# Kernel optimization log

Measured on AMD Instinct MI355X. Metric: run time of the kernel, lower is better.

The kernel has to match this reference:

```python
import jax, jax.numpy as jnp
import numpy as np

NEG_SLOPE = 0.01  # torch nn.LeakyReLU default
K_NN = 3          # PyG knn_interpolate default


def lrelu(v):
    return jax.nn.leaky_relu(v, NEG_SLOPE)


def mpl(x, ei, We, be, Wn, bn_):
    # MeshGraphNets-style message passing: edge MLP on [x_src||x_dst],
    # sum-aggregate at dst, node MLP on [x||agg].
    src, dst = ei[0], ei[1]
    m = lrelu(jnp.concatenate([x[src], x[dst]], axis=-1) @ We + be)   # [E, Co]
    agg = jax.ops.segment_sum(m, dst, num_segments=x.shape[0])        # [N, Co]
    return lrelu(jnp.concatenate([x, agg], axis=-1) @ Wn + bn_)


def knn_interpolate(x_c, pos_c, pos_f):
    # PyG knn_interpolate: inverse-squared-distance weighted k-NN average.
    d2 = jnp.sum((pos_f[:, None, :] - pos_c[None, :, :]) ** 2, axis=-1)  # [Nf, Nc]
    neg_d2, idx = jax.lax.top_k(-d2, K_NN)                               # [Nf, k]
    w = 1.0 / (-neg_d2 + 1e-16)
    xg = x_c[idx]                                                        # [Nf, k, C]
    return jnp.sum(w[..., None] * xg, axis=1) / jnp.sum(w, axis=1, keepdims=True)


def batch_norm(x, gamma, beta, eps=1e-5):
    # training-mode BatchNorm over the flattened node dim (PyG BatchNorm)
    mu = x.mean(axis=0)
    var = x.var(axis=0)
    return (x - mu) * jax.lax.rsqrt(var + eps) * gamma + beta


def setup_inputs() -> dict:
    key = jax.random.key(0)
    ks = jax.random.split(key, 20)
    B, Nc, Nf, D = 4, 2048, 8192, 3
    Cin, Cout = 128, 128
    Ch = Cout // 2
    Ec, Ef = 16384, 65536

    def w(k, shape):
        return jax.random.normal(k, shape, jnp.float32) / np.float32(np.sqrt(shape[0]))

    inp = {
        "x": jax.random.normal(ks[0], (B, Nc, Cin), jnp.float32),
        "weights": jax.random.uniform(ks[1], (B, Nc, 1), dtype=jnp.float32),
        "pos": jax.random.uniform(ks[2], (B, Nf, D), dtype=jnp.float32),
        # mpl1: Cin -> Cout//2 (coarse graph)
        "W1e": w(ks[3], (2 * Cin, Ch)), "b1e": jnp.zeros((Ch,), jnp.float32),
        "W1n": w(ks[4], (Cin + Ch, Ch)), "b1n": jnp.zeros((Ch,), jnp.float32),
        # mpl2: Cout//2 -> Cout (fine graph)
        "W2e": w(ks[5], (2 * Ch, Cout)), "b2e": jnp.zeros((Cout,), jnp.float32),
        "W2n": w(ks[6], (Ch + Cout, Cout)), "b2n": jnp.zeros((Cout,), jnp.float32),
        # mpl_skip: Cin -> Cout (fine graph)
        "Wse": w(ks[7], (2 * Cin, Cout)), "bse": jnp.zeros((Cout,), jnp.float32),
        "Wsn": w(ks[8], (Cin + Cout, Cout)), "bsn": jnp.zeros((Cout,), jnp.float32),
        "gamma": jnp.ones((Cout,), jnp.float32),
        "beta": jnp.zeros((Cout,), jnp.float32),
        # mask: indices of coarse nodes inside the fine node set (disjoint per graph)
        "mask": jnp.arange(B * Nc, dtype=jnp.int32).reshape(B, Nc),
        "e_coarse": jax.random.randint(ks[9], (B, 2, Ec), 0, Nc, jnp.int32),
        "e_fine": jax.random.randint(ks[10], (B, 2, Ef), 0, Nf, jnp.int32),
    }
    return inp


def reference(x, weights, pos, W1e, b1e, W1n, b1n, W2e, b2e, W2n, b2n,
              Wse, bse, Wsn, bsn, gamma, beta, mask, e_coarse, e_fine):
    B, Nf, _ = pos.shape

    def per_graph(xg, wg, posg, mg, ec, ef):
        pos_c = posg[mg]                                   # coarse positions
        # skip branch: up-pool then message passing on fine graph
        x_up = knn_interpolate(xg, pos_c, posg)            # [Nf, Cin]
        x_skip = mpl(x_up, ef, Wse, bse, Wsn, bsn)         # [Nf, Cout]
        # main branch: mpl on coarse graph, up-pool, mpl on fine graph
        x1 = mpl(xg, ec, W1e, b1e, W1n, b1n)               # [Nc, Cout//2]
        x1_up = knn_interpolate(x1, pos_c, posg)           # [Nf, Cout//2]
        x2 = mpl(x1_up, ef, W2e, b2e, W2n, b2n)            # [Nf, Cout]
        # Unpool node weights (scatter into zeros at mask rows)
        w_fine = jnp.zeros((Nf, wg.shape[-1]), wg.dtype).at[mg].set(wg)
        return x2 + x_skip, w_fine

    xs, w_fine = jax.vmap(per_graph)(x, weights, pos, mask, e_coarse, e_fine)
    C = xs.shape[-1]
    y = lrelu(batch_norm(xs.reshape(-1, C), gamma, beta)).reshape(xs.shape)
    return y, w_fine
```

## Files before the change

### kernel.cpp

```cpp
#include <hip/hip_runtime.h>
#include <hip/hip_bf16.h>
#include <cfloat>

#define B 4
#define NC 2048
#define NF 8192
#define CIN 128
#define CH 64
#define COUT 128
#define EC 16384
#define EF 65536
#define ZB 256

typedef __attribute__((ext_vector_type(8))) short short8v;
typedef __attribute__((ext_vector_type(4))) float f32x4;

__device__ __forceinline__ ushort f2b(float v) {
    __hip_bfloat16 h = __float2bfloat16(v);
    return *reinterpret_cast<ushort*>(&h);
}
__device__ __forceinline__ float b2f(ushort u) {
    __hip_bfloat16 h = *reinterpret_cast<__hip_bfloat16*>(&u);
    return __bfloat162float(h);
}

__global__ void count_all(const int* __restrict__ ec, const int* __restrict__ ef,
                          const int* __restrict__ mask, const float* __restrict__ pos,
                          int* __restrict__ cntC, int* __restrict__ cntF, int* __restrict__ cntZ,
                          int* __restrict__ inv,
                          const float* __restrict__ W2e, const float* __restrict__ W2n,
                          const float* __restrict__ Wse, const float* __restrict__ Wsn,
                          ushort* __restrict__ W2eT, ushort* __restrict__ W2nT,
                          ushort* __restrict__ WseT, ushort* __restrict__ WsnT) {
    const int b = blockIdx.y, z = blockIdx.z;
    const int i = blockIdx.x * 256 + threadIdx.x;
    if (z == 0) {
        if (i < EC) atomicAdd(&cntC[b * NC + ec[(size_t)b * 2 * EC + EC + i]], 1);
    } else if (z == 1) {
        if (i < EF) atomicAdd(&cntF[b * NF + ef[(size_t)b * 2 * EF + EF + i]], 1);
        if (i < NF) inv[(size_t)b * NF + i] = -1;
    } else if (z == 2) {
        if (i < NC) {
            int m = mask[b * NC + i];
            float pz = pos[((size_t)b * NF + m) * 3 + 2];
            int zb = min(max((int)(pz * (float)ZB), 0), ZB - 1);
            atomicAdd(&cntZ[b * ZB + zb], 1);
        }
    } else {
        const float* src; ushort* dst; int K2;
        switch (b) {
            case 0: src = W2e; dst = W2eT; K2 = 128; break;
            case 1: src = W2n; dst = W2nT; K2 = 192; break;
            case 2: src = Wse; dst = WseT; K2 = 256; break;
            default: src = Wsn; dst = WsnT; K2 = 256; break;
        }
        if (i < K2 * 128) {
            int n = i & 127, k = i >> 7;
            dst[(size_t)n * K2 + k] = f2b(src[i]);
        }
    }
}

template<int N, int OSTR, bool EXTRA>
__device__ __forceinline__ void scan_body(const int* __restrict__ cnt, int* __restrict__ offs,
                                          int* __restrict__ cur, int b, int* part) {
    const int tid = threadIdx.x;
    constexpr int PER = (N + 1023) / 1024;
    int local[PER];
    int s = 0;
    #pragma unroll
    for (int i = 0; i < PER; ++i) {
        int id = tid * PER + i;
        local[i] = s;
        if (id < N) s += cnt[b * N + id];
    }
    part[tid] = s;
    __syncthreads();
    for (int off = 1; off < 1024; off <<= 1) {
        int v = (tid >= off) ? part[tid - off] : 0;
        __syncthreads();
        part[tid] += v;
        __syncthreads();
    }
    int pre = tid ? part[tid - 1] : 0;
    #pragma unroll
    for (int i = 0; i < PER; ++i) {
        int id = tid * PER + i;
        if (id < N) {
            int o = pre + local[i];
            offs[b * OSTR + id] = o;
            cur[b * OSTR + id] = o;
        }
    }
    if (EXTRA && tid == 1023) offs[b * OSTR + N] = part[1023];
}

__global__ __launch_bounds__(1024) void scan_all(
    const int* __restrict__ cntC, int* __restrict__ offC, int* __restrict__ curC,
    const int* __restrict__ cntF, int* __restrict__ offF, int* __restrict__ curF,
    const int* __restrict__ cntZ, int* __restrict__ offZ, int* __restrict__ curZ) {
    __shared__ int part[1024];
    const int cfg = blockIdx.x >> 2;
    const int b = blockIdx.x & 3;
    if (cfg == 0)      scan_body<NC, NC, false>(cntC, offC, curC, b, part);
    else if (cfg == 1) scan_body<NF, NF, false>(cntF, offF, curF, b, part);
    else               scan_body<ZB, ZB + 1, true>(cntZ, offZ, curZ, b, part);
}

__global__ void fill_all(const int* __restrict__ ec, const int* __restrict__ ef,
                         const int* __restrict__ mask, const float* __restrict__ pos,
                         int* __restrict__ curC, int* __restrict__ curF, int* __restrict__ curZ,
                         int* __restrict__ csrC, int* __restrict__ csrF,
                         float4* __restrict__ sposg, int* __restrict__ inv) {
    const int b = blockIdx.y, z = blockIdx.z;
    const int i = blockIdx.x * 256 + threadIdx.x;
    if (z == 0) {
        if (i < EC) {
            const int* eb = ec + (size_t)b * 2 * EC;
            int src = eb[i], dst = eb[EC + i];
            int p = atomicAdd(&curC[b * NC + dst], 1);
            csrC[(size_t)b * EC + p] = src;
        }
    } else if (z == 1) {
        if (i < EF) {
            const int* eb = ef + (size_t)b * 2 * EF;
            int src = eb[i], dst = eb[EF + i];
            int p = atomicAdd(&curF[b * NF + dst], 1);
            csrF[(size_t)b * EF + p] = src;
        }
    } else {
        if (i < NC) {
            int m = mask[b * NC + i];
            const float* p = pos + ((size_t)b * NF + m) * 3;
            float px = p[0], py = p[1], pz = p[2];
            int zb = min(max((int)(pz * (float)ZB), 0), ZB - 1);
            int slot = atomicAdd(&curZ[b * (ZB + 1) + zb], 1);
            sposg[(size_t)b * NC + slot] = make_float4(px, py, pz, __int_as_float(i));
            inv[(size_t)b * NF + m] = b * NC + i;
        }
    }
}

__device__ __forceinline__ void ins3(float d, int c, float& d0, float& d1, float& d2,
                                     int& i0, int& i1, int& i2) {
    bool lt0 = d < d0, lt1 = d < d1, lt2 = d < d2;
    d2 = lt1 ? d1 : (lt2 ? d : d2);  i2 = lt1 ? i1 : (lt2 ? c : i2);
    d1 = lt0 ? d0 : (lt1 ? d : d1);  i1 = lt0 ? i0 : (lt1 ? c : i1);
    d0 = lt0 ? d  : d0;              i0 = lt0 ? c  : i0;
}
__device__ __forceinline__ void merge32(float& d0, float& d1, float& d2,
                                        int& i0, int& i1, int& i2) {
    #pragma unroll
    for (int off = 1; off <= 16; off <<= 1) {
        float od[3]; int oi[3];
        od[0] = __shfl_xor(d0, off); oi[0] = __shfl_xor(i0, off);
        od[1] = __shfl_xor(d1, off); oi[1] = __shfl_xor(i1, off);
        od[2] = __shfl_xor(d2, off); oi[2] = __shfl_xor(i2, off);
        #pragma unroll
        for (int j = 0; j < 3; ++j) ins3(od[j], oi[j], d0, d1, d2, i0, i1, i2);
    }
}

__global__ __launch_bounds__(256) void knn_interp(const float* __restrict__ pos,
                                                  const float4* __restrict__ sposg,
                                                  const int* __restrict__ offZ,
                                                  const float* __restrict__ xc,
                                                  int* __restrict__ idx,
                                                  float* __restrict__ wn,
                                                  ushort* __restrict__ xup) {
    const int b = blockIdx.y;
    const int tid = threadIdx.x;
    const int node = blockIdx.x * 8 + (tid >> 5);
    const int lane = tid & 31;
    const float* pf = pos + ((size_t)b * NF + node) * 3;
    const float px = pf[0], py = pf[1], pz = pf[2];
    const float4* sp = sposg + (size_t)b * NC;
    const int zb = min(max((int)(pz * (float)ZB), 0), ZB - 1);
    const int zlo = max(zb - 32, 0), zhi = min(zb + 32, ZB - 1);
    const int j0 = offZ[b * (ZB + 1) + zlo];
    const int j1 = offZ[b * (ZB + 1) + zhi + 1];
    float d0 = FLT_MAX, d1 = FLT_MAX, d2 = FLT_MAX;
    int i0 = 0, i1 = 0, i2 = 0;
    for (int j = j0 + lane; j < j1; j += 32) {
        float4 s = sp[j];
        float ddx = __fsub_rn(px, s.x);
        float ddy = __fsub_rn(py, s.y);
        float ddz = __fsub_rn(pz, s.z);
        float d = __fadd_rn(__fadd_rn(__fmul_rn(ddx, ddx), __fmul_rn(ddy, ddy)),
                            __fmul_rn(ddz, ddz));
        ins3(d, __float_as_int(s.w), d0, d1, d2, i0, i1, i2);
    }
    merge32(d0, d1, d2, i0, i1, i2);
    float bd = 1e30f;
    if (zlo > 0)      bd = fminf(bd, pz - (float)zlo * (1.0f / ZB));
    if (zhi < ZB - 1) bd = fminf(bd, (float)(zhi + 1) * (1.0f / ZB) - pz);
    bd *= 0.9999f;
    if (__any(d2 > bd * bd)) {
        d0 = d1 = d2 = FLT_MAX; i0 = i1 = i2 = 0;
        for (int j = lane; j < NC; j += 32) {
            float4 s = sp[j];
            float ddx = __fsub_rn(px, s.x);
            float ddy = __fsub_rn(py, s.y);
            float ddz = __fsub_rn(pz, s.z);
            float d = __fadd_rn(__fadd_rn(__fmul_rn(ddx, ddx), __fmul_rn(ddy, ddy)),
                                __fmul_rn(ddz, ddz));
            ins3(d, __float_as_int(s.w), d0, d1, d2, i0, i1, i2);
        }
        merge32(d0, d1, d2, i0, i1, i2);
    }
    float w0 = 1.0f / (d0 + 1e-16f);
    float w1 = 1.0f / (d1 + 1e-16f);
    float w2 = 1.0f / (d2 + 1e-16f);
    float inv = 1.0f / (w0 + w1 + w2);
    w0 *= inv; w1 *= inv; w2 *= inv;
    if (lane == 0) {
        size_t o = ((size_t)b * NF + node) * 3;
        idx[o] = i0; idx[o + 1] = i1; idx[o + 2] = i2;
        wn[o] = w0; wn[o + 1] = w1; wn[o + 2] = w2;
    }
    const float* xb = xc + (size_t)b * NC * CIN;
    float4 a = *(const float4*)&xb[(size_t)i0 * CIN + lane * 4];
    float4 bb = *(const float4*)&xb[(size_t)i1 * CIN + lane * 4];
    float4 cc = *(const float4*)&xb[(size_t)i2 * CIN + lane * 4];
    ushort4 u;
    u.x = f2b(w0 * a.x + w1 * bb.x + w2 * cc.x);
    u.y = f2b(w0 * a.y + w1 * bb.y + w2 * cc.y);
    u.z = f2b(w0 * a.z + w1 * bb.z + w2 * cc.z);
    u.w = f2b(w0 * a.w + w1 * bb.w + w2 * cc.w);
    *(ushort4*)&xup[((size_t)b * NF + node) * CIN + lane * 4] = u;
}

template<int S>
__global__ __launch_bounds__(256) void interp_b16(const float* __restrict__ xc,
                                                  const int* __restrict__ idx,
                                                  const float* __restrict__ wn,
                                                  ushort* __restrict__ out) {
    constexpr int C = 4 << S;
    const int b = blockIdx.y;
    const int node = blockIdx.x * (256 >> S) + (threadIdx.x >> S);
    const int lane = threadIdx.x & ((1 << S) - 1);
    size_t o = ((size_t)b * NF + node) * 3;
    int i0 = idx[o], i1 = idx[o + 1], i2 = idx[o + 2];
    float w0 = wn[o], w1 = wn[o + 1], w2 = wn[o + 2];
    const float* xb = xc + (size_t)b * NC * C;
    float4 a = *(const float4*)&xb[(size_t)i0 * C + lane * 4];
    float4 bb = *(const float4*)&xb[(size_t)i1 * C + lane * 4];
    float4 cc = *(const float4*)&xb[(size_t)i2 * C + lane * 4];
    ushort4 u;
    u.x = f2b(w0 * a.x + w1 * bb.x + w2 * cc.x);
    u.y = f2b(w0 * a.y + w1 * bb.y + w2 * cc.y);
    u.z = f2b(w0 * a.z + w1 * bb.z + w2 * cc.z);
    u.w = f2b(w0 * a.w + w1 * bb.w + w2 * cc.w);
    *(ushort4*)&out[((size_t)b * NF + node) * C + lane * 4] = u;
}

__global__ __launch_bounds__(256) void gemm_kernel(
    const float* __restrict__ A1, int K1, const float* __restrict__ A2, int K2,
    const float* __restrict__ W, const float* __restrict__ bias,
    float* __restrict__ Cmat, int M, int N, int flags,
    long sA1, long sA2, long sC) {
    __shared__ float As[16][64];
    __shared__ float Wsh[16][64];
    const int b = blockIdx.z;
    const int m0 = blockIdx.y * 64, n0 = blockIdx.x * 64;
    const int t = threadIdx.x;
    const int tx = t & 15, ty = t >> 4;
    float acc[4][4] = {};
    int kOff = 0;
    for (int s = 0; s < 2; ++s) {
        const float* A = (s == 0) ? A1 : A2;
        const int K = (s == 0) ? K1 : K2;
        const long sA = (s == 0) ? sA1 : sA2;
        if (A == nullptr || K == 0) continue;
        const float* Ab = A + (size_t)b * sA;
        const int lm = t >> 2;
        const int lk = (t & 3) << 2;
        const int wk = t >> 4;
        const int wng = (t & 15) << 2;
        for (int k0 = 0; k0 < K; k0 += 16) {
            float4 av = *(const float4*)&Ab[(size_t)(m0 + lm) * K + k0 + lk];
            As[lk + 0][lm] = av.x; As[lk + 1][lm] = av.y;
            As[lk + 2][lm] = av.z; As[lk + 3][lm] = av.w;
            float4 wv = *(const float4*)&W[(size_t)(kOff + k0 + wk) * N + n0 + wng];
            *(float4*)&Wsh[wk][wng] = wv;
            __syncthreads();
            #pragma unroll
            for (int k = 0; k < 16; ++k) {
                float4 a4 = *(const float4*)&As[k][ty << 2];
                float4 w4 = *(const float4*)&Wsh[k][tx << 2];
                float aa[4] = {a4.x, a4.y, a4.z, a4.w};
                float ww[4] = {w4.x, w4.y, w4.z, w4.w};
                #pragma unroll
                for (int i = 0; i < 4; ++i)
                    #pragma unroll
                    for (int j = 0; j < 4; ++j)
                        acc[i][j] = fmaf(aa[i], ww[j], acc[i][j]);
            }
            __syncthreads();
        }
        kOff += K;
    }
    float* Cb = Cmat + (size_t)b * sC;
    #pragma unroll
    for (int i = 0; i < 4; ++i) {
        int m = m0 + (ty << 2) + i;
        #pragma unroll
        for (int j = 0; j < 4; ++j) {
            int n = n0 + (tx << 2) + j;
            float v = acc[i][j];
            if (bias) v += bias[n];
            if (flags & 1) v = v > 0.0f ? v : 0.01f * v;
            float* cp = &Cb[(size_t)m * N + n];
            if (flags & 2) v += *cp;
            *cp = v;
        }
    }
}

__global__ __launch_bounds__(256) void gemm_pq64(const float* __restrict__ x,
                                                 const float* __restrict__ W1e,
                                                 float* __restrict__ Pb,
                                                 float* __restrict__ Qb) {
    __shared__ float As[16][64];
    __shared__ float Wsh[16][64];
    const int z = blockIdx.z;
    const int b = z >> 1, pq = z & 1;
    const int m0 = blockIdx.x * 64;
    const float* Ab = x + (size_t)b * NC * CIN;
    const float* W = W1e + pq * CIN * CH;
    float* Cb = (pq ? Qb : Pb) + (size_t)b * NC * CH;
    const int t = threadIdx.x;
    const int tx = t & 15, ty = t >> 4;
    const int lm = t >> 2, lk = (t & 3) << 2;
    const int wk = t >> 4, wng = (t & 15) << 2;
    float acc[4][4] = {};
    for (int k0 = 0; k0 < CIN; k0 += 16) {
        float4 av = *(const float4*)&Ab[(size_t)(m0 + lm) * CIN + k0 + lk];
        As[lk + 0][lm] = av.x; As[lk + 1][lm] = av.y;
        As[lk + 2][lm] = av.z; As[lk + 3][lm] = av.w;
        float4 wv = *(const float4*)&W[(size_t)(k0 + wk) * CH + wng];
        *(float4*)&Wsh[wk][wng] = wv;
        __syncthreads();
        #pragma unroll
        for (int k = 0; k < 16; ++k) {
            float4 a4 = *(const float4*)&As[k][ty << 2];
            float4 w4 = *(const float4*)&Wsh[k][tx << 2];
            float aa[4] = {a4.x, a4.y, a4.z, a4.w};
            float ww[4] = {w4.x, w4.y, w4.z, w4.w};
            #pragma unroll
            for (int i = 0; i < 4; ++i)
                #pragma unroll
                for (int j = 0; j < 4; ++j)
                    acc[i][j] = fmaf(aa[i], ww[j], acc[i][j]);
        }
        __syncthreads();
    }
    #pragma unroll
    for (int i = 0; i < 4; ++i) {
        int m = m0 + (ty << 2) + i;
        #pragma unroll
        for (int j = 0; j < 4; ++j)
            Cb[(size_t)m * CH + (tx << 2) + j] = acc[i][j];
    }
}

#define LDK 40
__device__ __forceinline__ void mfma_seg(const ushort* __restrict__ Ab, int K, int m0,
                                         const ushort* __restrict__ Wt, int ldW, int wcol0,
                                         ushort* As, ushort* Wsm,
                                         int t, int wr, int wc, int fr, int fq,
                                         f32x4 (&acc)[4][4]) {
    const int sr = t >> 2, sk = (t & 3) * 8;
    for (int k0 = 0; k0 < K; k0 += 32) {
        #pragma unroll
        for (int p = 0; p < 2; ++p) {
            int r = sr + p * 64;
            *reinterpret_cast<int4*>(&As[r * LDK + sk]) =
                *reinterpret_cast<const int4*>(&Ab[(size_t)(m0 + r) * K + k0 + sk]);
            *reinterpret_cast<int4*>(&Wsm[r * LDK + sk]) =
                *reinterpret_cast<const int4*>(&Wt[(size_t)r * ldW + wcol0 + k0 + sk]);
        }
        __syncthreads();
        short8v af[4], wf[4];
        #pragma unroll
        for (int m = 0; m < 4; ++m)
            af[m] = *reinterpret_cast<const short8v*>(&As[(wr * 64 + m * 16 + fr) * LDK + fq * 8]);
        #pragma unroll
        for (int n = 0; n < 4; ++n)
            wf[n] = *reinterpret_cast<const short8v*>(&Wsm[(wc * 64 + n * 16 + fr) * LDK + fq * 8]);
        #pragma unroll
        for (int m = 0; m < 4; ++m)
            #pragma unroll
            for (int n = 0; n < 4; ++n)
                acc[m][n] = __builtin_amdgcn_mfma_f32_16x16x32_bf16(af[m], wf[n], acc[m][n], 0, 0, 0);
        __syncthreads();
    }
}

__global__ __launch_bounds__(256) void mfma_pq_fused(
    const ushort* __restrict__ x1upb, const ushort* __restrict__ xupb,
    const ushort* __restrict__ W2eT, const ushort* __restrict__ WseT,
    ushort* __restrict__ P2, ushort* __restrict__ Q2,
    ushort* __restrict__ PS, ushort* __restrict__ QS) {
    __shared__ ushort As[128 * LDK];
    __shared__ ushort Ws0[128 * LDK];
    __shared__ ushort Ws1[128 * LDK];
    const int t = threadIdx.x;
    const int lane = t & 63, wid = t >> 6;
    const int wr = wid >> 1, wc = wid & 1;
    const int fr = lane & 15, fq = lane >> 4;
    const int sr = t >> 2, sk = (t & 3) * 8;
    const int z = blockIdx.z;
    const int b = z >> 1, br = z & 1;
    const int m0 = blockIdx.x * 128;
    const ushort* Ab = br ? xupb + (size_t)b * NF * 128 : x1upb + (size_t)b * NF * 64;
    const int K = br ? 128 : 64;
    const ushort* Wt = br ? WseT : W2eT;
    const int ldW = br ? 256 : 128;
    f32x4 accP[4][4], accQ[4][4];
    #pragma unroll
    for (int m = 0; m < 4; ++m)
        #pragma unroll
        for (int n = 0; n < 4; ++n) {
            accP[m][n] = (f32x4){0.f, 0.f, 0.f, 0.f};
            accQ[m][n] = (f32x4){0.f, 0.f, 0.f, 0.f};
        }
    for (int k0 = 0; k0 < K; k0 += 32) {
        #pragma unroll
        for (int p = 0; p < 2; ++p) {
            int r = sr + p * 64;
            *reinterpret_cast<int4*>(&As[r * LDK + sk]) =
                *reinterpret_cast<const int4*>(&Ab[(size_t)(m0 + r) * K + k0 + sk]);
            *reinterpret_cast<int4*>(&Ws0[r * LDK + sk]) =
                *reinterpret_cast<const int4*>(&Wt[(size_t)r * ldW + k0 + sk]);
            *reinterpret_cast<int4*>(&Ws1[r * LDK + sk]) =
                *reinterpret_cast<const int4*>(&Wt[(size_t)r * ldW + K + k0 + sk]);
        }
        __syncthreads();
        short8v af[4], w0[4], w1[4];
        #pragma unroll
        for (int m = 0; m < 4; ++m)
            af[m] = *reinterpret_cast<const short8v*>(&As[(wr * 64 + m * 16 + fr) * LDK + fq * 8]);
        #pragma unroll
        for (int n = 0; n < 4; ++n) {
            w0[n] = *reinterpret_cast<const short8v*>(&Ws0[(wc * 64 + n * 16 + fr) * LDK + fq * 8]);
            w1[n] = *reinterpret_cast<const short8v*>(&Ws1[(wc * 64 + n * 16 + fr) * LDK + fq * 8]);
        }
        #pragma unroll
        for (int m = 0; m < 4; ++m)
            #pragma unroll
            for (int n = 0; n < 4; ++n) {
                accP[m][n] = __builtin_amdgcn_mfma_f32_16x16x32_bf16(af[m], w0[n], accP[m][n], 0, 0, 0);
                accQ[m][n] = __builtin_amdgcn_mfma_f32_16x16x32_bf16(af[m], w1[n], accQ[m][n], 0, 0, 0);
            }
        __syncthreads();
    }
    ushort* Pb = (br ? PS : P2) + (size_t)b * NF * 128;
    ushort* Qb = (br ? QS : Q2) + (size_t)b * NF * 128;
    #pragma unroll
    for (int m = 0; m < 4; ++m)
        #pragma unroll
        for (int n = 0; n < 4; ++n) {
            int col = wc * 64 + n * 16 + fr;
            #pragma unroll
            for (int r = 0; r < 4; ++r) {
                int row = m0 + wr * 64 + m * 16 + fq * 4 + r;
                Pb[(size_t)row * 128 + col] = f2b(accP[m][n][r]);
                Qb[(size_t)row * 128 + col] = f2b(accQ[m][n][r]);
            }
        }
}

__global__ __launch_bounds__(256) void mfma_node2(
    const ushort* __restrict__ A1, const ushort* __restrict__ A2,
    const ushort* __restrict__ Wt1, const float* __restrict__ bias1,
    const ushort* __restrict__ A3, const ushort* __restrict__ A4,
    const ushort* __restrict__ Wt2, const float* __restrict__ bias2,
    float* __restrict__ y, float* __restrict__ stats) {
    __shared__ ushort As[128 * LDK];
    __shared__ ushort Wsm[128 * LDK];
    const int t = threadIdx.x;
    const int lane = t & 63, wid = t >> 6;
    const int wr = wid >> 1, wc = wid & 1;
    const int fr = lane & 15, fq = lane >> 4;
    const int b = blockIdx.z;
    const int m0 = blockIdx.x * 128;
    f32x4 acc1[4][4], acc2[4][4];
    #pragma unroll
    for (int m = 0; m < 4; ++m)
        #pragma unroll
        for (int n = 0; n < 4; ++n) {
            acc1[m][n] = (f32x4){0.f, 0.f, 0.f, 0.f};
            acc2[m][n] = (f32x4){0.f, 0.f, 0.f, 0.f};
        }
    mfma_seg(A1 + (size_t)b * NF * 64,  64,  m0, Wt1, 192, 0,   As, Wsm, t, wr, wc, fr, fq, acc1);
    mfma_seg(A2 + (size_t)b * NF * 128, 128, m0, Wt1, 192, 64,  As, Wsm, t, wr, wc, fr, fq, acc1);
    mfma_seg(A3 + (size_t)b * NF * 128, 128, m0, Wt2, 256, 0,   As, Wsm, t, wr, wc, fr, fq, acc2);
    mfma_seg(A4 + (size_t)b * NF * 128, 128, m0, Wt2, 256, 128, As, Wsm, t, wr, wc, fr, fq, acc2);
    float* Yb = y + (size_t)b * NF * 128;
    float lsum[4] = {0.f, 0.f, 0.f, 0.f}, lsq[4] = {0.f, 0.f, 0.f, 0.f};
    #pragma unroll
    for (int m = 0; m < 4; ++m)
        #pragma unroll
        for (int n = 0; n < 4; ++n) {
            int col = wc * 64 + n * 16 + fr;
            float bv1 = bias1[col], bv2 = bias2[col];
            #pragma unroll
            for (int r = 0; r < 4; ++r) {
                int row = m0 + wr * 64 + m * 16 + fq * 4 + r;
                float v1 = acc1[m][n][r] + bv1; v1 = v1 > 0.0f ? v1 : 0.01f * v1;
                float v2 = acc2[m][n][r] + bv2; v2 = v2 > 0.0f ? v2 : 0.01f * v2;
                float v = v1 + v2;
                Yb[(size_t)row * 128 + col] = v;
                lsum[n] += v;
                lsq[n] = fmaf(v, v, lsq[n]);
            }
        }
    __syncthreads();
    float* ssum = reinterpret_cast<float*>(As);
    float* ssq  = ssum + 128;
    if (t < 128) { ssum[t] = 0.0f; ssq[t] = 0.0f; }
    __syncthreads();
    #pragma unroll
    for (int n = 0; n < 4; ++n) {
        int col = wc * 64 + n * 16 + fr;
        atomicAdd(&ssum[col], lsum[n]);
        atomicAdd(&ssq[col], lsq[n]);
    }
    __syncthreads();
    if (t < 128) {
        atomicAdd(&stats[t], ssum[t]);
        atomicAdd(&stats[128 + t], ssq[t]);
    }
}

__global__ __launch_bounds__(256) void agg_csr_f32(const float* __restrict__ P,
                                                   const float* __restrict__ Q,
                                                   const float* __restrict__ bias,
                                                   const int* __restrict__ offs,
                                                   const int* __restrict__ counts,
                                                   const int* __restrict__ csr_src,
                                                   float* __restrict__ agg,
                                                   int N, int E) {
    const int b = blockIdx.y;
    const int dst = blockIdx.x * 4 + (threadIdx.x >> 6);
    const int lane = threadIdx.x & 63;
    const float* Pb = P + (size_t)b * N * 64;
    const float* Qb = Q + (size_t)b * N * 64;
    const int start = offs[b * N + dst];
    const int cnt = counts[b * N + dst];
    const int* sl = csr_src + (size_t)b * E + start;
    const float q = Qb[(size_t)dst * 64 + lane] + bias[lane];
    float a = 0.0f;
    for (int i = 0; i < cnt; ++i) {
        int src = sl[i];
        float m = Pb[(size_t)src * 64 + lane] + q; m = m > 0.0f ? m : 0.01f * m;
        a += m;
    }
    agg[(size_t)b * N * 64 + (size_t)dst * 64 + lane] = a;
}

__global__ __launch_bounds__(256) void agg_csr_b16(const ushort* __restrict__ P2,
                                                   const ushort* __restrict__ Q2,
                                                   const float* __restrict__ b2,
                                                   const ushort* __restrict__ PS,
                                                   const ushort* __restrict__ QS,
                                                   const float* __restrict__ bS,
                                                   const int* __restrict__ offs,
                                                   const int* __restrict__ counts,
                                                   const int* __restrict__ csr_src,
                                                   ushort* __restrict__ agg2,
                                                   ushort* __restrict__ aggS) {
    const int lin = blockIdx.x;
    const int pair = lin & 7;
    const int b = pair >> 1, br = pair & 1;
    const int chunk = lin >> 3;
    const ushort* P = br ? PS : P2;
    const ushort* Q = br ? QS : Q2;
    const float* bias = br ? bS : b2;
    ushort* agg = br ? aggS : agg2;
    const int dst = chunk * 4 + (threadIdx.x >> 6);
    const int lane = threadIdx.x & 63;
    const ushort* Pb = P + (size_t)b * NF * 128;
    const ushort* Qb = Q + (size_t)b * NF * 128;
    const int start = offs[b * NF + dst];
    const int cnt = counts[b * NF + dst];
    const int* sl = csr_src + (size_t)b * EF + start;
    const int c0 = lane, c1 = lane + 64;
    const float q0 = b2f(Qb[(size_t)dst * 128 + c0]) + bias[c0];
    const float q1 = b2f(Qb[(size_t)dst * 128 + c1]) + bias[c1];
    float a0 = 0.0f, a1 = 0.0f;
    int i = 0;
    for (; i + 4 <= cnt; i += 4) {
        int s0 = sl[i], s1 = sl[i + 1], s2 = sl[i + 2], s3 = sl[i + 3];
        ushort p00 = Pb[(size_t)s0 * 128 + c0], p01 = Pb[(size_t)s0 * 128 + c1];
        ushort p10 = Pb[(size_t)s1 * 128 + c0], p11 = Pb[(size_t)s1 * 128 + c1];
        ushort p20 = Pb[(size_t)s2 * 128 + c0], p21 = Pb[(size_t)s2 * 128 + c1];
        ushort p30 = Pb[(size_t)s3 * 128 + c0], p31 = Pb[(size_t)s3 * 128 + c1];
        float m;
        m = b2f(p00) + q0; m = m > 0.0f ? m : 0.01f * m; a0 += m;
        m = b2f(p01) + q1; m = m > 0.0f ? m : 0.01f * m; a1 += m;
        m = b2f(p10) + q0; m = m > 0.0f ? m : 0.01f * m; a0 += m;
        m = b2f(p11) + q1; m = m > 0.0f ? m : 0.01f * m; a1 += m;
        m = b2f(p20) + q0; m = m > 0.0f ? m : 0.01f * m; a0 += m;
        m = b2f(p21) + q1; m = m > 0.0f ? m : 0.01f * m; a1 += m;
        m = b2f(p30) + q0; m = m > 0.0f ? m : 0.01f * m; a0 += m;
        m = b2f(p31) + q1; m = m > 0.0f ? m : 0.01f * m; a1 += m;
    }
    for (; i < cnt; ++i) {
        int src = sl[i];
        float m0 = b2f(Pb[(size_t)src * 128 + c0]) + q0; m0 = m0 > 0.0f ? m0 : 0.01f * m0;
        float m1 = b2f(Pb[(size_t)src * 128 + c1]) + q1; m1 = m1 > 0.0f ? m1 : 0.01f * m1;
        a0 += m0; a1 += m1;
    }
    __builtin_nontemporal_store(f2b(a0), &agg[(size_t)b * NF * 128 + (size_t)dst * 128 + c0]);
    __builtin_nontemporal_store(f2b(a1), &agg[(size_t)b * NF * 128 + (size_t)dst * 128 + c1]);
}

__global__ __launch_bounds__(256) void bn_final(float* __restrict__ xs,
                                                const float* __restrict__ stats,
                                                const float* __restrict__ gamma,
                                                const float* __restrict__ beta,
                                                float* __restrict__ wf,
                                                const float* __restrict__ wts,
                                                const int* __restrict__ inv) {
    const long i = (long)blockIdx.x * 256 + threadIdx.x;
    const long g4 = i * 4;
    const int c = (int)(g4 & (COUT - 1));
    const float invN = 1.0f / (float)(B * NF);
    float4 v = *(float4*)&xs[g4];
    float vv[4] = {v.x, v.y, v.z, v.w};
    #pragma unroll
    for (int k = 0; k < 4; ++k) {
        int ck = c + k;
        float mu = stats[ck] * invN;
        float var = stats[COUT + ck] * invN - mu * mu;
        float t = (vv[k] - mu) * rsqrtf(var + 1e-5f) * gamma[ck] + beta[ck];
        vv[k] = t > 0.0f ? t : 0.01f * t;
    }
    *(float4*)&xs[g4] = make_float4(vv[0], vv[1], vv[2], vv[3]);
    if (i < (long)B * NF) {
        int iv = inv[i];
        wf[i] = (iv >= 0) ? wts[iv] : 0.0f;
    }
}

extern "C" void kernel_launch(void* const* d_in, const int* in_sizes, int n_in,
                              void* d_out, int out_size, void* d_ws, size_t ws_size,
                              hipStream_t stream) {
    const float* x    = (const float*)d_in[0];
    const float* wts  = (const float*)d_in[1];
    const float* pos  = (const float*)d_in[2];
    const float* W1e  = (const float*)d_in[3];
    const float* b1e  = (const float*)d_in[4];
    const float* W1n  = (const float*)d_in[5];
    const float* b1n  = (const float*)d_in[6];
    const float* W2e  = (const float*)d_in[7];
    const float* b2e  = (const float*)d_in[8];
    const float* W2n  = (const float*)d_in[9];
    const float* b2n  = (const float*)d_in[10];
    const float* Wse  = (const float*)d_in[11];
    const float* bse  = (const float*)d_in[12];
    const float* Wsn  = (const float*)d_in[13];
    const float* bsn  = (const float*)d_in[14];
    const float* gamma= (const float*)d_in[15];
    const float* beta = (const float*)d_in[16];
    const int*   mask = (const int*)d_in[17];
    const int*   ec   = (const int*)d_in[18];
    const int*   ef   = (const int*)d_in[19];

    float* ws = (float*)d_ws;
    int*    idxb  = (int*)ws;
    float*  wnb   = ws + 98304;
    float4* sposg = (float4*)(ws + 196608);
    float*  x1    = ws + 196608 + 32768;
    float*  PbC   = x1  + (size_t)B * NC * CH;
    float*  QbC   = PbC + (size_t)B * NC * CH;
    float*  aggC  = QbC + (size_t)B * NC * CH;
    float*  stats = aggC+ (size_t)B * NC * CH;
    int* cntC  = (int*)(stats + 256);
    int* cntF  = cntC + B * NC;
    int* cntZ  = cntF + B * NF;
    int* offC  = cntZ + B * ZB;
    int* curC  = offC + B * NC;
    int* offF  = curC + B * NC;
    int* curF  = offF + B * NF;
    int* offZ  = curF + B * NF;
    int* curZ  = offZ + B * (ZB + 1);
    int* csrC  = curZ + B * (ZB + 1);
    int* csrF  = csrC + B * EC;
    int* invm  = csrF + B * EF;
    size_t foff = (size_t)(invm + (size_t)B * NF - (int*)ws);
    foff = (foff + 7) & ~(size_t)7;
    ushort* xupb  = (ushort*)(ws + foff);
    ushort* x1upb = xupb  + (size_t)B * NF * 128;
    ushort* P2b   = x1upb + (size_t)B * NF * 64;
    ushort* Q2b   = P2b   + (size_t)B * NF * 128;
    ushort* PSb   = Q2b   + (size_t)B * NF * 128;
    ushort* QSb   = PSb   + (size_t)B * NF * 128;
    ushort* agg2b = QSb   + (size_t)B * NF * 128;
    ushort* aggSb = agg2b + (size_t)B * NF * 128;
    ushort* W2eT  = aggSb + (size_t)B * NF * 128;
    ushort* W2nT  = W2eT  + 128 * 128;
    ushort* WseT  = W2nT  + 128 * 192;
    ushort* WsnT  = WseT  + 128 * 256;

    float* y  = (float*)d_out;
    float* wf = y + (size_t)B * NF * COUT;

    hipMemsetAsync(stats, 0, 256 * 4 + (size_t)B * (NC + NF + ZB) * 4, stream);
    count_all<<<dim3(EF / 256, B, 4), 256, 0, stream>>>(
        ec, ef, mask, pos, cntC, cntF, cntZ, invm,
        W2e, W2n, Wse, Wsn, W2eT, W2nT, WseT, WsnT);
    scan_all<<<dim3(3 * B), 1024, 0, stream>>>(cntC, offC, curC, cntF, offF, curF, cntZ, offZ, curZ);
    fill_all<<<dim3(EF / 256, B, 3), 256, 0, stream>>>(ec, ef, mask, pos, curC, curF, curZ,
                                                       csrC, csrF, sposg, invm);

    knn_interp<<<dim3(NF / 8, B), 256, 0, stream>>>(pos, sposg, offZ, x, idxb, wnb, xupb);

    gemm_pq64<<<dim3(NC / 64, 1, B * 2), 256, 0, stream>>>(x, W1e, PbC, QbC);
    agg_csr_f32<<<dim3(NC / 4, B), 256, 0, stream>>>(
        PbC, QbC, b1e, offC, cntC, csrC, aggC, NC, EC);
    gemm_kernel<<<dim3(1, NC / 64, B), 256, 0, stream>>>(
        x, CIN, aggC, CH, W1n, b1n, x1, NC, CH, 1, (long)NC * CIN, (long)NC * CH, (long)NC * CH);

    interp_b16<4><<<dim3(NF / 16, B), 256, 0, stream>>>(x1, idxb, wnb, x1upb);

    mfma_pq_fused<<<dim3(NF / 128, 1, B * 2), 256, 0, stream>>>(
        x1upb, xupb, W2eT, WseT, P2b, Q2b, PSb, QSb);
    agg_csr_b16<<<dim3((NF / 4) * B * 2), 256, 0, stream>>>(
        P2b, Q2b, b2e, PSb, QSb, bse, offF, cntF, csrF, agg2b, aggSb);

    mfma_node2<<<dim3(NF / 128, 1, B), 256, 0, stream>>>(
        x1upb, agg2b, W2nT, b2n, xupb, aggSb, WsnT, bsn, y, stats);

    bn_final<<<dim3((long)B * NF * COUT / 1024), 256, 0, stream>>>(y, stats, gamma, beta, wf, wts, invm);
}
```

Baseline: 198.3 us.

## Move coarse-graph GEMMs to bf16 MFMA and co-schedule branches in merged launches

The coarse-graph edge and node GEMMs switch from fp32 SIMT kernels to bf16 MFMA tiles, using weights and x converted to bf16 during the setup kernel. Independent work from the skip and main branches is packed into shared launches: knn with the coarse PQ GEMM, skip PQ GEMM with coarse aggregation, and coarse node GEMM with skip aggregation. Intermediates such as x1 are now stored in bf16. This cuts launch count and serial dependency gaps and fills the device better. The cost is more bf16 rounding on the coarse path and branch divergence between block roles inside each kernel.

```diff
diff --git a/kernel.cpp b/kernel.cpp
--- a/kernel.cpp
+++ b/kernel.cpp
@@ -11,6 +11,7 @@
 #define EC 16384
 #define EF 65536
 #define ZB 256
+#define LDK 40
 
 typedef __attribute__((ext_vector_type(8))) short short8v;
 typedef __attribute__((ext_vector_type(4))) float f32x4;
@@ -31,7 +32,10 @@
                           const float* __restrict__ W2e, const float* __restrict__ W2n,
                           const float* __restrict__ Wse, const float* __restrict__ Wsn,
                           ushort* __restrict__ W2eT, ushort* __restrict__ W2nT,
-                          ushort* __restrict__ WseT, ushort* __restrict__ WsnT) {
+                          ushort* __restrict__ WseT, ushort* __restrict__ WsnT,
+                          const float* __restrict__ W1e, const float* __restrict__ W1n,
+                          ushort* __restrict__ W1eT, ushort* __restrict__ W1nT,
+                          const float* __restrict__ x, ushort* __restrict__ xb16) {
     const int b = blockIdx.y, z = blockIdx.z;
     const int i = blockIdx.x * 256 + threadIdx.x;
     if (z == 0) {
@@ -46,7 +50,7 @@
             int zb = min(max((int)(pz * (float)ZB), 0), ZB - 1);
             atomicAdd(&cntZ[b * ZB + zb], 1);
         }
-    } else {
+    } else if (z == 3) {
         const float* src; ushort* dst; int K2;
         switch (b) {
             case 0: src = W2e; dst = W2eT; K2 = 128; break;
@@ -58,6 +62,21 @@
             int n = i & 127, k = i >> 7;
             dst[(size_t)n * K2 + k] = f2b(src[i]);
         }
+    } else if (z == 4) {
+        if (b == 0) {
+            if (i < 128 * 128) {
+                int n = i >> 7, k = i & 127;
+                W1eT[i] = f2b(W1e[(size_t)(k + ((n >> 6) << 7)) * 64 + (n & 63)]);
+            }
+        } else if (b == 1) {
+            if (i < 64 * 192) {
+                int n = i / 192, k = i - n * 192;
+                W1nT[i] = f2b(W1n[(size_t)k * 64 + n]);
+            }
+        }
+    } else {
+        for (int j = i; j < NC * CIN; j += (EF / 256) * 256)
+            xb16[(size_t)b * NC * CIN + j] = f2b(x[(size_t)b * NC * CIN + j]);
     }
 }
 
@@ -161,16 +180,81 @@
     }
 }
 
-__global__ __launch_bounds__(256) void knn_interp(const float* __restrict__ pos,
-                                                  const float4* __restrict__ sposg,
-                                                  const int* __restrict__ offZ,
-                                                  const float* __restrict__ xc,
-                                                  int* __restrict__ idx,
-                                                  float* __restrict__ wn,
-                                                  ushort* __restrict__ xup) {
-    const int b = blockIdx.y;
+__device__ __forceinline__ void mfma_seg(const ushort* __restrict__ Ab, int K, int m0,
+                                         const ushort* __restrict__ Wt, int ldW, int wcol0,
+                                         ushort* As, ushort* Wsm,
+                                         int t, int wr, int wc, int fr, int fq,
+                                         f32x4 (&acc)[4][4]) {
+    const int sr = t >> 2, sk = (t & 3) * 8;
+    for (int k0 = 0; k0 < K; k0 += 32) {
+        #pragma unroll
+        for (int p = 0; p < 2; ++p) {
+            int r = sr + p * 64;
+            *reinterpret_cast<int4*>(&As[r * LDK + sk]) =
+                *reinterpret_cast<const int4*>(&Ab[(size_t)(m0 + r) * K + k0 + sk]);
+            *reinterpret_cast<int4*>(&Wsm[r * LDK + sk]) =
+                *reinterpret_cast<const int4*>(&Wt[(size_t)r * ldW + wcol0 + k0 + sk]);
+        }
+        __syncthreads();
+        short8v af[4], wf[4];
+        #pragma unroll
+        for (int m = 0; m < 4; ++m)
+            af[m] = *reinterpret_cast<const short8v*>(&As[(wr * 64 + m * 16 + fr) * LDK + fq * 8]);
+        #pragma unroll
+        for (int n = 0; n < 4; ++n)
+            wf[n] = *reinterpret_cast<const short8v*>(&Wsm[(wc * 64 + n * 16 + fr) * LDK + fq * 8]);
+        #pragma unroll
+        for (int m = 0; m < 4; ++m)
+            #pragma unroll
+            for (int n = 0; n < 4; ++n)
+                acc[m][n] = __builtin_amdgcn_mfma_f32_16x16x32_bf16(af[m], wf[n], acc[m][n], 0, 0, 0);
+        __syncthreads();
+    }
+}
+
+__global__ __launch_bounds__(256) void knn_cpq(const float* __restrict__ pos,
+                                               const float4* __restrict__ sposg,
+                                               const int* __restrict__ offZ,
+                                               const float* __restrict__ xc,
+                                               int* __restrict__ idx,
+                                               float* __restrict__ wn,
+                                               ushort* __restrict__ xup,
+                                               const ushort* __restrict__ xb16,
+                                               const ushort* __restrict__ W1eT,
+                                               ushort* __restrict__ PQc) {
+    __shared__ ushort As[128 * LDK];
+    __shared__ ushort Wsm[128 * LDK];
+    const int bx = blockIdx.x;
     const int tid = threadIdx.x;
-    const int node = blockIdx.x * 8 + (tid >> 5);
+    if (bx < B * NC / 128) {
+        const int b = bx >> 4, m0 = (bx & 15) * 128;
+        const int lane = tid & 63, wid = tid >> 6;
+        const int wr = wid >> 1, wc = wid & 1;
+        const int fr = lane & 15, fq = lane >> 4;
+        f32x4 acc[4][4];
+        #pragma unroll
+        for (int m = 0; m < 4; ++m)
+            #pragma unroll
+            for (int n = 0; n < 4; ++n) acc[m][n] = (f32x4){0.f, 0.f, 0.f, 0.f};
+        mfma_seg(xb16 + (size_t)b * NC * 128, 128, m0, W1eT, 128, 0,
+                 As, Wsm, tid, wr, wc, fr, fq, acc);
+        ushort* Cb = PQc + (size_t)b * NC * 128;
+        #pragma unroll
+        for (int m = 0; m < 4; ++m)
+            #pragma unroll
+            for (int n = 0; n < 4; ++n) {
+                int col = wc * 64 + n * 16 + fr;
+                #pragma unroll
+                for (int r = 0; r < 4; ++r) {
+                    int row = m0 + wr * 64 + m * 16 + fq * 4 + r;
+                    Cb[(size_t)row * 128 + col] = f2b(acc[m][n][r]);
+                }
+            }
+        return;
+    }
+    const int t2 = bx - B * NC / 128;
+    const int b = t2 >> 10;
+    const int node = (t2 & 1023) * 8 + (tid >> 5);
     const int lane = tid & 31;
     const float* pf = pos + ((size_t)b * NF + node) * 3;
     const float px = pf[0], py = pf[1], pz = pf[2];
@@ -230,193 +314,14 @@
     *(ushort4*)&xup[((size_t)b * NF + node) * CIN + lane * 4] = u;
 }
 
-template<int S>
-__global__ __launch_bounds__(256) void interp_b16(const float* __restrict__ xc,
-                                                  const int* __restrict__ idx,
-                                                  const float* __restrict__ wn,
-                                                  ushort* __restrict__ out) {
-    constexpr int C = 4 << S;
-    const int b = blockIdx.y;
-    const int node = blockIdx.x * (256 >> S) + (threadIdx.x >> S);
-    const int lane = threadIdx.x & ((1 << S) - 1);
-    size_t o = ((size_t)b * NF + node) * 3;
-    int i0 = idx[o], i1 = idx[o + 1], i2 = idx[o + 2];
-    float w0 = wn[o], w1 = wn[o + 1], w2 = wn[o + 2];
-    const float* xb = xc + (size_t)b * NC * C;
-    float4 a = *(const float4*)&xb[(size_t)i0 * C + lane * 4];
-    float4 bb = *(const float4*)&xb[(size_t)i1 * C + lane * 4];
-    float4 cc = *(const float4*)&xb[(size_t)i2 * C + lane * 4];
-    ushort4 u;
-    u.x = f2b(w0 * a.x + w1 * bb.x + w2 * cc.x);
-    u.y = f2b(w0 * a.y + w1 * bb.y + w2 * cc.y);
-    u.z = f2b(w0 * a.z + w1 * bb.z + w2 * cc.z);
-    u.w = f2b(w0 * a.w + w1 * bb.w + w2 * cc.w);
-    *(ushort4*)&out[((size_t)b * NF + node) * C + lane * 4] = u;
-}
-
-__global__ __launch_bounds__(256) void gemm_kernel(
-    const float* __restrict__ A1, int K1, const float* __restrict__ A2, int K2,
-    const float* __restrict__ W, const float* __restrict__ bias,
-    float* __restrict__ Cmat, int M, int N, int flags,
-    long sA1, long sA2, long sC) {
-    __shared__ float As[16][64];
-    __shared__ float Wsh[16][64];
-    const int b = blockIdx.z;
-    const int m0 = blockIdx.y * 64, n0 = blockIdx.x * 64;
-    const int t = threadIdx.x;
-    const int tx = t & 15, ty = t >> 4;
-    float acc[4][4] = {};
-    int kOff = 0;
-    for (int s = 0; s < 2; ++s) {
-        const float* A = (s == 0) ? A1 : A2;
-        const int K = (s == 0) ? K1 : K2;
-        const long sA = (s == 0) ? sA1 : sA2;
-        if (A == nullptr || K == 0) continue;
-        const float* Ab = A + (size_t)b * sA;
-        const int lm = t >> 2;
-        const int lk = (t & 3) << 2;
-        const int wk = t >> 4;
-        const int wng = (t & 15) << 2;
-        for (int k0 = 0; k0 < K; k0 += 16) {
-            float4 av = *(const float4*)&Ab[(size_t)(m0 + lm) * K + k0 + lk];
-            As[lk + 0][lm] = av.x; As[lk + 1][lm] = av.y;
-            As[lk + 2][lm] = av.z; As[lk + 3][lm] = av.w;
-            float4 wv = *(const float4*)&W[(size_t)(kOff + k0 + wk) * N + n0 + wng];
-            *(float4*)&Wsh[wk][wng] = wv;
-            __syncthreads();
-            #pragma unroll
-            for (int k = 0; k < 16; ++k) {
-                float4 a4 = *(const float4*)&As[k][ty << 2];
-                float4 w4 = *(const float4*)&Wsh[k][tx << 2];
-                float aa[4] = {a4.x, a4.y, a4.z, a4.w};
-                float ww[4] = {w4.x, w4.y, w4.z, w4.w};
-                #pragma unroll
-                for (int i = 0; i < 4; ++i)
-                    #pragma unroll
-                    for (int j = 0; j < 4; ++j)
-                        acc[i][j] = fmaf(aa[i], ww[j], acc[i][j]);
-            }
-            __syncthreads();
-        }
-        kOff += K;
-    }
-    float* Cb = Cmat + (size_t)b * sC;
-    #pragma unroll
-    for (int i = 0; i < 4; ++i) {
-        int m = m0 + (ty << 2) + i;
-        #pragma unroll
-        for (int j = 0; j < 4; ++j) {
-            int n = n0 + (tx << 2) + j;
-            float v = acc[i][j];
-            if (bias) v += bias[n];
-            if (flags & 1) v = v > 0.0f ? v : 0.01f * v;
-            float* cp = &Cb[(size_t)m * N + n];
-            if (flags & 2) v += *cp;
-            *cp = v;
-        }
-    }
-}
-
-__global__ __launch_bounds__(256) void gemm_pq64(const float* __restrict__ x,
-                                                 const float* __restrict__ W1e,
-                                                 float* __restrict__ Pb,
-                                                 float* __restrict__ Qb) {
-    __shared__ float As[16][64];
-    __shared__ float Wsh[16][64];
-    const int z = blockIdx.z;
-    const int b = z >> 1, pq = z & 1;
-    const int m0 = blockIdx.x * 64;
-    const float* Ab = x + (size_t)b * NC * CIN;
-    const float* W = W1e + pq * CIN * CH;
-    float* Cb = (pq ? Qb : Pb) + (size_t)b * NC * CH;
-    const int t = threadIdx.x;
-    const int tx = t & 15, ty = t >> 4;
-    const int lm = t >> 2, lk = (t & 3) << 2;
-    const int wk = t >> 4, wng = (t & 15) << 2;
-    float acc[4][4] = {};
-    for (int k0 = 0; k0 < CIN; k0 += 16) {
-        float4 av = *(const float4*)&Ab[(size_t)(m0 + lm) * CIN + k0 + lk];
-        As[lk + 0][lm] = av.x; As[lk + 1][lm] = av.y;
-        As[lk + 2][lm] = av.z; As[lk + 3][lm] = av.w;
-        float4 wv = *(const float4*)&W[(size_t)(k0 + wk) * CH + wng];
-        *(float4*)&Wsh[wk][wng] = wv;
-        __syncthreads();
-        #pragma unroll
-        for (int k = 0; k < 16; ++k) {
-            float4 a4 = *(const float4*)&As[k][ty << 2];
-            float4 w4 = *(const float4*)&Wsh[k][tx << 2];
-            float aa[4] = {a4.x, a4.y, a4.z, a4.w};
-            float ww[4] = {w4.x, w4.y, w4.z, w4.w};
-            #pragma unroll
-            for (int i = 0; i < 4; ++i)
-                #pragma unroll
-                for (int j = 0; j < 4; ++j)
-                    acc[i][j] = fmaf(aa[i], ww[j], acc[i][j]);
-        }
-        __syncthreads();
-    }
-    #pragma unroll
-    for (int i = 0; i < 4; ++i) {
-        int m = m0 + (ty << 2) + i;
-        #pragma unroll
-        for (int j = 0; j < 4; ++j)
-            Cb[(size_t)m * CH + (tx << 2) + j] = acc[i][j];
-    }
-}
-
-#define LDK 40
-__device__ __forceinline__ void mfma_seg(const ushort* __restrict__ Ab, int K, int m0,
-                                         const ushort* __restrict__ Wt, int ldW, int wcol0,
-                                         ushort* As, ushort* Wsm,
-                                         int t, int wr, int wc, int fr, int fq,
-                                         f32x4 (&acc)[4][4]) {
-    const int sr = t >> 2, sk = (t & 3) * 8;
-    for (int k0 = 0; k0 < K; k0 += 32) {
-        #pragma unroll
-        for (int p = 0; p < 2; ++p) {
-            int r = sr + p * 64;
-            *reinterpret_cast<int4*>(&As[r * LDK + sk]) =
-                *reinterpret_cast<const int4*>(&Ab[(size_t)(m0 + r) * K + k0 + sk]);
-            *reinterpret_cast<int4*>(&Wsm[r * LDK + sk]) =
-                *reinterpret_cast<const int4*>(&Wt[(size_t)r * ldW + wcol0 + k0 + sk]);
-        }
-        __syncthreads();
-        short8v af[4], wf[4];
-        #pragma unroll
-        for (int m = 0; m < 4; ++m)
-            af[m] = *reinterpret_cast<const short8v*>(&As[(wr * 64 + m * 16 + fr) * LDK + fq * 8]);
-        #pragma unroll
-        for (int n = 0; n < 4; ++n)
-            wf[n] = *reinterpret_cast<const short8v*>(&Wsm[(wc * 64 + n * 16 + fr) * LDK + fq * 8]);
-        #pragma unroll
-        for (int m = 0; m < 4; ++m)
-            #pragma unroll
-            for (int n = 0; n < 4; ++n)
-                acc[m][n] = __builtin_amdgcn_mfma_f32_16x16x32_bf16(af[m], wf[n], acc[m][n], 0, 0, 0);
-        __syncthreads();
-    }
-}
-
-__global__ __launch_bounds__(256) void mfma_pq_fused(
-    const ushort* __restrict__ x1upb, const ushort* __restrict__ xupb,
-    const ushort* __restrict__ W2eT, const ushort* __restrict__ WseT,
-    ushort* __restrict__ P2, ushort* __restrict__ Q2,
-    ushort* __restrict__ PS, ushort* __restrict__ QS) {
-    __shared__ ushort As[128 * LDK];
-    __shared__ ushort Ws0[128 * LDK];
-    __shared__ ushort Ws1[128 * LDK];
-    const int t = threadIdx.x;
+__device__ __forceinline__ void pq_body(const ushort* __restrict__ Ab, int K,
+                                        const ushort* __restrict__ Wt, int ldW, int m0,
+                                        ushort* __restrict__ Pb, ushort* __restrict__ Qb,
+                                        int t, ushort* As, ushort* Ws0, ushort* Ws1) {
     const int lane = t & 63, wid = t >> 6;
     const int wr = wid >> 1, wc = wid & 1;
     const int fr = lane & 15, fq = lane >> 4;
     const int sr = t >> 2, sk = (t & 3) * 8;
-    const int z = blockIdx.z;
-    const int b = z >> 1, br = z & 1;
-    const int m0 = blockIdx.x * 128;
-    const ushort* Ab = br ? xupb + (size_t)b * NF * 128 : x1upb + (size_t)b * NF * 64;
-    const int K = br ? 128 : 64;
-    const ushort* Wt = br ? WseT : W2eT;
-    const int ldW = br ? 256 : 128;
     f32x4 accP[4][4], accQ[4][4];
     #pragma unroll
     for (int m = 0; m < 4; ++m)
@@ -455,8 +360,6 @@
             }
         __syncthreads();
     }
-    ushort* Pb = (br ? PS : P2) + (size_t)b * NF * 128;
-    ushort* Qb = (br ? QS : Q2) + (size_t)b * NF * 128;
     #pragma unroll
     for (int m = 0; m < 4; ++m)
         #pragma unroll
@@ -471,121 +374,10 @@
         }
 }
 
-__global__ __launch_bounds__(256) void mfma_node2(
-    const ushort* __restrict__ A1, const ushort* __restrict__ A2,
-    const ushort* __restrict__ Wt1, const float* __restrict__ bias1,
-    const ushort* __restrict__ A3, const ushort* __restrict__ A4,
-    const ushort* __restrict__ Wt2, const float* __restrict__ bias2,
-    float* __restrict__ y, float* __restrict__ stats) {
-    __shared__ ushort As[128 * LDK];
-    __shared__ ushort Wsm[128 * LDK];
-    const int t = threadIdx.x;
-    const int lane = t & 63, wid = t >> 6;
-    const int wr = wid >> 1, wc = wid & 1;
-    const int fr = lane & 15, fq = lane >> 4;
-    const int b = blockIdx.z;
-    const int m0 = blockIdx.x * 128;
-    f32x4 acc1[4][4], acc2[4][4];
-    #pragma unroll
-    for (int m = 0; m < 4; ++m)
-        #pragma unroll
-        for (int n = 0; n < 4; ++n) {
-            acc1[m][n] = (f32x4){0.f, 0.f, 0.f, 0.f};
-            acc2[m][n] = (f32x4){0.f, 0.f, 0.f, 0.f};
-        }
-    mfma_seg(A1 + (size_t)b * NF * 64,  64,  m0, Wt1, 192, 0,   As, Wsm, t, wr, wc, fr, fq, acc1);
-    mfma_seg(A2 + (size_t)b * NF * 128, 128, m0, Wt1, 192, 64,  As, Wsm, t, wr, wc, fr, fq, acc1);
-    mfma_seg(A3 + (size_t)b * NF * 128, 128, m0, Wt2, 256, 0,   As, Wsm, t, wr, wc, fr, fq, acc2);
-    mfma_seg(A4 + (size_t)b * NF * 128, 128, m0, Wt2, 256, 128, As, Wsm, t, wr, wc, fr, fq, acc2);
-    float* Yb = y + (size_t)b * NF * 128;
-    float lsum[4] = {0.f, 0.f, 0.f, 0.f}, lsq[4] = {0.f, 0.f, 0.f, 0.f};
-    #pragma unroll
-    for (int m = 0; m < 4; ++m)
-        #pragma unroll
-        for (int n = 0; n < 4; ++n) {
-            int col = wc * 64 + n * 16 + fr;
-            float bv1 = bias1[col], bv2 = bias2[col];
-            #pragma unroll
-            for (int r = 0; r < 4; ++r) {
-                int row = m0 + wr * 64 + m * 16 + fq * 4 + r;
-                float v1 = acc1[m][n][r] + bv1; v1 = v1 > 0.0f ? v1 : 0.01f * v1;
-                float v2 = acc2[m][n][r] + bv2; v2 = v2 > 0.0f ? v2 : 0.01f * v2;
-                float v = v1 + v2;
-                Yb[(size_t)row * 128 + col] = v;
-                lsum[n] += v;
-                lsq[n] = fmaf(v, v, lsq[n]);
-            }
-        }
-    __syncthreads();
-    float* ssum = reinterpret_cast<float*>(As);
-    float* ssq  = ssum + 128;
-    if (t < 128) { ssum[t] = 0.0f; ssq[t] = 0.0f; }
-    __syncthreads();
-    #pragma unroll
-    for (int n = 0; n < 4; ++n) {
-        int col = wc * 64 + n * 16 + fr;
-        atomicAdd(&ssum[col], lsum[n]);
-        atomicAdd(&ssq[col], lsq[n]);
-    }
-    __syncthreads();
-    if (t < 128) {
-        atomicAdd(&stats[t], ssum[t]);
-        atomicAdd(&stats[128 + t], ssq[t]);
-    }
-}
-
-__global__ __launch_bounds__(256) void agg_csr_f32(const float* __restrict__ P,
-                                                   const float* __restrict__ Q,
-                                                   const float* __restrict__ bias,
-                                                   const int* __restrict__ offs,
-                                                   const int* __restrict__ counts,
-                                                   const int* __restrict__ csr_src,
-                                                   float* __restrict__ agg,
-                                                   int N, int E) {
-    const int b = blockIdx.y;
-    const int dst = blockIdx.x * 4 + (threadIdx.x >> 6);
-    const int lane = threadIdx.x & 63;
-    const float* Pb = P + (size_t)b * N * 64;
-    const float* Qb = Q + (size_t)b * N * 64;
-    const int start = offs[b * N + dst];
-    const int cnt = counts[b * N + dst];
-    const int* sl = csr_src + (size_t)b * E + start;
-    const float q = Qb[(size_t)dst * 64 + lane] + bias[lane];
-    float a = 0.0f;
-    for (int i = 0; i < cnt; ++i) {
-        int src = sl[i];
-        float m = Pb[(size_t)src * 64 + lane] + q; m = m > 0.0f ? m : 0.01f * m;
-        a += m;
-    }
-    agg[(size_t)b * N * 64 + (size_t)dst * 64 + lane] = a;
-}
-
-__global__ __launch_bounds__(256) void agg_csr_b16(const ushort* __restrict__ P2,
-                                                   const ushort* __restrict__ Q2,
-                                                   const float* __restrict__ b2,
-                                                   const ushort* __restrict__ PS,
-                                                   const ushort* __restrict__ QS,
-                                                   const float* __restrict__ bS,
-                                                   const int* __restrict__ offs,
-                                                   const int* __restrict__ counts,
-                                                   const int* __restrict__ csr_src,
-                                                   ushort* __restrict__ agg2,
-                                                   ushort* __restrict__ aggS) {
-    const int lin = blockIdx.x;
-    const int pair = lin & 7;
-    const int b = pair >> 1, br = pair & 1;
-    const int chunk = lin >> 3;
-    const ushort* P = br ? PS : P2;
-    const ushort* Q = br ? QS : Q2;
-    const float* bias = br ? bS : b2;
-    ushort* agg = br ? aggS : agg2;
-    const int dst = chunk * 4 + (threadIdx.x >> 6);
-    const int lane = threadIdx.x & 63;
-    const ushort* Pb = P + (size_t)b * NF * 128;
-    const ushort* Qb = Q + (size_t)b * NF * 128;
-    const int start = offs[b * NF + dst];
-    const int cnt = counts[b * NF + dst];
-    const int* sl = csr_src + (size_t)b * EF + start;
+__device__ __forceinline__ void agg_fine(const ushort* __restrict__ Pb, const ushort* __restrict__ Qb,
+                                         const float* __restrict__ bias, int start, int cnt,
+                                         const int* __restrict__ sl, ushort* __restrict__ aggRow,
+                                         int dst, int lane) {
     const int c0 = lane, c1 = lane + 64;
     const float q0 = b2f(Qb[(size_t)dst * 128 + c0]) + bias[c0];
     const float q1 = b2f(Qb[(size_t)dst * 128 + c1]) + bias[c1];
@@ -613,8 +405,263 @@
         float m1 = b2f(Pb[(size_t)src * 128 + c1]) + q1; m1 = m1 > 0.0f ? m1 : 0.01f * m1;
         a0 += m0; a1 += m1;
     }
-    __builtin_nontemporal_store(f2b(a0), &agg[(size_t)b * NF * 128 + (size_t)dst * 128 + c0]);
-    __builtin_nontemporal_store(f2b(a1), &agg[(size_t)b * NF * 128 + (size_t)dst * 128 + c1]);
+    __builtin_nontemporal_store(f2b(a0), &aggRow[(size_t)dst * 128 + c0]);
+    __builtin_nontemporal_store(f2b(a1), &aggRow[(size_t)dst * 128 + c1]);
+}
+
+__global__ __launch_bounds__(256) void pqs_aggc(const ushort* __restrict__ xupb,
+                                                const ushort* __restrict__ WseT,
+                                                ushort* __restrict__ PS, ushort* __restrict__ QS,
+                                                const ushort* __restrict__ PQc,
+                                                const float* __restrict__ b1e,
+                                                const int* __restrict__ offC,
+                                                const int* __restrict__ cntC,
+                                                const int* __restrict__ csrC,
+                                                ushort* __restrict__ aggC) {
+    __shared__ ushort As[128 * LDK];
+    __shared__ ushort Ws0[128 * LDK];
+    __shared__ ushort Ws1[128 * LDK];
+    const int bx = blockIdx.x;
+    const int tid = threadIdx.x;
+    if (bx < B * NF / 128) {
+        const int b = bx >> 6, m0 = (bx & 63) * 128;
+        pq_body(xupb + (size_t)b * NF * 128, 128, WseT, 256, m0,
+                PS + (size_t)b * NF * 128, QS + (size_t)b * NF * 128, tid, As, Ws0, Ws1);
+        return;
+    }
+    const int t2 = bx - B * NF / 128;
+    const int b = t2 >> 9;
+    const int dst = (t2 & 511) * 4 + (tid >> 6);
+    const int lane = tid & 63;
+    const ushort* Pb = PQc + (size_t)b * NC * 128;
+    const int start = offC[b * NC + dst];
+    const int cnt = cntC[b * NC + dst];
+    const int* sl = csrC + (size_t)b * EC + start;
+    const float q = b2f(Pb[(size_t)dst * 128 + 64 + lane]) + b1e[lane];
+    float a = 0.0f;
+    for (int i = 0; i < cnt; ++i) {
+        int src = sl[i];
+        float m = b2f(Pb[(size_t)src * 128 + lane]) + q; m = m > 0.0f ? m : 0.01f * m;
+        a += m;
+    }
+    aggC[(size_t)b * NC * 64 + (size_t)dst * 64 + lane] = f2b(a);
+}
+
+__global__ __launch_bounds__(256) void x1_aggs(const ushort* __restrict__ xb16,
+                                               const ushort* __restrict__ aggC,
+                                               const ushort* __restrict__ W1nT,
+                                               const float* __restrict__ b1n,
+                                               ushort* __restrict__ x1b,
+                                               const ushort* __restrict__ PS,
+                                               const ushort* __restrict__ QS,
+                                               const float* __restrict__ bse,
+                                               const int* __restrict__ offF,
+                                               const int* __restrict__ cntF,
+                                               const int* __restrict__ csrF,
+                                               ushort* __restrict__ aggS) {
+    __shared__ ushort As[256 * LDK];
+    __shared__ ushort Wsm[64 * LDK];
+    const int bx = blockIdx.x;
+    const int tid = threadIdx.x;
+    if (bx < B * NC / 256) {
+        const int b = bx >> 3, m0 = (bx & 7) * 256;
+        const int lane = tid & 63, wr = tid >> 6;
+        const int fr = lane & 15, fq = lane >> 4;
+        const int sr = tid >> 2, sk = (tid & 3) * 8;
+        f32x4 acc[4][4];
+        #pragma unroll
+        for (int m = 0; m < 4; ++m)
+            #pragma unroll
+            for (int n = 0; n < 4; ++n) acc[m][n] = (f32x4){0.f, 0.f, 0.f, 0.f};
+        const ushort* A1 = xb16 + (size_t)b * NC * 128;
+        for (int k0 = 0; k0 < 128; k0 += 32) {
+            #pragma unroll
+            for (int p = 0; p < 4; ++p) {
+                int r = sr + p * 64;
+                *reinterpret_cast<int4*>(&As[r * LDK + sk]) =
+                    *reinterpret_cast<const int4*>(&A1[(size_t)(m0 + r) * 128 + k0 + sk]);
+            }
+            *reinterpret_cast<int4*>(&Wsm[sr * LDK + sk]) =
+                *reinterpret_cast<const int4*>(&W1nT[(size_t)sr * 192 + k0 + sk]);
+            __syncthreads();
+            short8v af[4], wf[4];
+            #pragma unroll
+            for (int m = 0; m < 4; ++m)
+                af[m] = *reinterpret_cast<const short8v*>(&As[(wr * 64 + m * 16 + fr) * LDK + fq * 8]);
+            #pragma unroll
+            for (int n = 0; n < 4; ++n)
+                wf[n] = *reinterpret_cast<const short8v*>(&Wsm[(n * 16 + fr) * LDK + fq * 8]);
+            #pragma unroll
+            for (int m = 0; m < 4; ++m)
+                #pragma unroll
+                for (int n = 0; n < 4; ++n)
+                    acc[m][n] = __builtin_amdgcn_mfma_f32_16x16x32_bf16(af[m], wf[n], acc[m][n], 0, 0, 0);
+            __syncthreads();
+        }
+        const ushort* A2 = aggC + (size_t)b * NC * 64;
+        for (int k0 = 0; k0 < 64; k0 += 32) {
+            #pragma unroll
+            for (int p = 0; p < 4; ++p) {
+                int r = sr + p * 64;
+                *reinterpret_cast<int4*>(&As[r * LDK + sk]) =
+                    *reinterpret_cast<const int4*>(&A2[(size_t)(m0 + r) * 64 + k0 + sk]);
+            }
+            *reinterpret_cast<int4*>(&Wsm[sr * LDK + sk]) =
+                *reinterpret_cast<const int4*>(&W1nT[(size_t)sr * 192 + 128 + k0 + sk]);
+            __syncthreads();
+            short8v af[4], wf[4];
+            #pragma unroll
+            for (int m = 0; m < 4; ++m)
+                af[m] = *reinterpret_cast<const short8v*>(&As[(wr * 64 + m * 16 + fr) * LDK + fq * 8]);
+            #pragma unroll
+            for (int n = 0; n < 4; ++n)
+                wf[n] = *reinterpret_cast<const short8v*>(&Wsm[(n * 16 + fr) * LDK + fq * 8]);
+            #pragma unroll
+            for (int m = 0; m < 4; ++m)
+                #pragma unroll
+                for (int n = 0; n < 4; ++n)
+                    acc[m][n] = __builtin_amdgcn_mfma_f32_16x16x32_bf16(af[m], wf[n], acc[m][n], 0, 0, 0);
+            __syncthreads();
+        }
+        ushort* Cb = x1b + (size_t)b * NC * 64;
+        #pragma unroll
+        for (int m = 0; m < 4; ++m)
+            #pragma unroll
+            for (int n = 0; n < 4; ++n) {
+                int col = n * 16 + fr;
+                float bv = b1n[col];
+                #pragma unroll
+                for (int r = 0; r < 4; ++r) {
+                    int row = m0 + wr * 64 + m * 16 + fq * 4 + r;
+                    float v = acc[m][n][r] + bv;
+                    v = v > 0.0f ? v : 0.01f * v;
+                    Cb[(size_t)row * 64 + col] = f2b(v);
+                }
+            }
+        return;
+    }
+    const int t2 = bx - B * NC / 256;
+    const int b = t2 & 3;
+    const int dst = (t2 >> 2) * 4 + (tid >> 6);
+    const int lane = tid & 63;
+    const int start = offF[b * NF + dst];
+    const int cnt = cntF[b * NF + dst];
+    agg_fine(PS + (size_t)b * NF * 128, QS + (size_t)b * NF * 128, bse, start, cnt,
+             csrF + (size_t)b * EF + start, aggS + (size_t)b * NF * 128, dst, lane);
+}
+
+__global__ __launch_bounds__(256) void interp_x1(const ushort* __restrict__ x1b,
+                                                 const int* __restrict__ idx,
+                                                 const float* __restrict__ wn,
+                                                 ushort* __restrict__ out) {
+    const int b = blockIdx.y;
+    const int node = blockIdx.x * 16 + (threadIdx.x >> 4);
+    const int lane = threadIdx.x & 15;
+    size_t o = ((size_t)b * NF + node) * 3;
+    int i0 = idx[o], i1 = idx[o + 1], i2 = idx[o + 2];
+    float w0 = wn[o], w1 = wn[o + 1], w2 = wn[o + 2];
+    const ushort* xb = x1b + (size_t)b * NC * 64;
+    ushort4 a = *(const ushort4*)&xb[(size_t)i0 * 64 + lane * 4];
+    ushort4 bb = *(const ushort4*)&xb[(size_t)i1 * 64 + lane * 4];
+    ushort4 cc = *(const ushort4*)&xb[(size_t)i2 * 64 + lane * 4];
+    ushort4 u;
+    u.x = f2b(w0 * b2f(a.x) + w1 * b2f(bb.x) + w2 * b2f(cc.x));
+    u.y = f2b(w0 * b2f(a.y) + w1 * b2f(bb.y) + w2 * b2f(cc.y));
+    u.z = f2b(w0 * b2f(a.z) + w1 * b2f(bb.z) + w2 * b2f(cc.z));
+    u.w = f2b(w0 * b2f(a.w) + w1 * b2f(bb.w) + w2 * b2f(cc.w));
+    *(ushort4*)&out[((size_t)b * NF + node) * 64 + lane * 4] = u;
+}
+
+__global__ __launch_bounds__(256) void pq2_kernel(const ushort* __restrict__ x1upb,
+                                                  const ushort* __restrict__ W2eT,
+                                                  ushort* __restrict__ P2, ushort* __restrict__ Q2) {
+    __shared__ ushort As[128 * LDK];
+    __shared__ ushort Ws0[128 * LDK];
+    __shared__ ushort Ws1[128 * LDK];
+    const int bx = blockIdx.x;
+    const int b = bx >> 6, m0 = (bx & 63) * 128;
+    pq_body(x1upb + (size_t)b * NF * 64, 64, W2eT, 128, m0,
+            P2 + (size_t)b * NF * 128, Q2 + (size_t)b * NF * 128, threadIdx.x, As, Ws0, Ws1);
+}
+
+__global__ __launch_bounds__(256) void agg2_kernel(const ushort* __restrict__ P2,
+                                                   const ushort* __restrict__ Q2,
+                                                   const float* __restrict__ b2e,
+                                                   const int* __restrict__ offF,
+                                                   const int* __restrict__ cntF,
+                                                   const int* __restrict__ csrF,
+                                                   ushort* __restrict__ agg2) {
+    const int bx = blockIdx.x;
+    const int b = bx & 3;
+    const int dst = (bx >> 2) * 4 + (threadIdx.x >> 6);
+    const int lane = threadIdx.x & 63;
+    const int start = offF[b * NF + dst];
+    const int cnt = cntF[b * NF + dst];
+    agg_fine(P2 + (size_t)b * NF * 128, Q2 + (size_t)b * NF * 128, b2e, start, cnt,
+             csrF + (size_t)b * EF + start, agg2 + (size_t)b * NF * 128, dst, lane);
+}
+
+__global__ __launch_bounds__(256) void mfma_node2(
+    const ushort* __restrict__ A1, const ushort* __restrict__ A2,
+    const ushort* __restrict__ Wt1, const float* __restrict__ bias1,
+    const ushort* __restrict__ A3, const ushort* __restrict__ A4,
+    const ushort* __restrict__ Wt2, const float* __restrict__ bias2,
+    float* __restrict__ y, float* __restrict__ stats) {
+    __shared__ ushort As[128 * LDK];
+    __shared__ ushort Wsm[128 * LDK];
+    const int t = threadIdx.x;
+    const int lane = t & 63, wid = t >> 6;
+    const int wr = wid >> 1, wc = wid & 1;
+    const int fr = lane & 15, fq = lane >> 4;
+    const int b = blockIdx.z;
+    const int m0 = blockIdx.x * 128;
+    f32x4 acc1[4][4], acc2[4][4];
+    #pragma unroll
+    for (int m = 0; m < 4; ++m)
+        #pragma unroll
+        for (int n = 0; n < 4; ++n) {
+            acc1[m][n] = (f32x4){0.f, 0.f, 0.f, 0.f};
+            acc2[m][n] = (f32x4){0.f, 0.f, 0.f, 0.f};
+        }
+    mfma_seg(A1 + (size_t)b * NF * 64,  64,  m0, Wt1, 192, 0,   As, Wsm, t, wr, wc, fr, fq, acc1);
+    mfma_seg(A2 + (size_t)b * NF * 128, 128, m0, Wt1, 192, 64,  As, Wsm, t, wr, wc, fr, fq, acc1);
+    mfma_seg(A3 + (size_t)b * NF * 128, 128, m0, Wt2, 256, 0,   As, Wsm, t, wr, wc, fr, fq, acc2);
+    mfma_seg(A4 + (size_t)b * NF * 128, 128, m0, Wt2, 256, 128, As, Wsm, t, wr, wc, fr, fq, acc2);
+    float* Yb = y + (size_t)b * NF * 128;
+    float lsum[4] = {0.f, 0.f, 0.f, 0.f}, lsq[4] = {0.f, 0.f, 0.f, 0.f};
+    #pragma unroll
+    for (int m = 0; m < 4; ++m)
+        #pragma unroll
+        for (int n = 0; n < 4; ++n) {
+            int col = wc * 64 + n * 16 + fr;
+            float bv1 = bias1[col], bv2 = bias2[col];
+            #pragma unroll
+            for (int r = 0; r < 4; ++r) {
+                int row = m0 + wr * 64 + m * 16 + fq * 4 + r;
+                float v1 = acc1[m][n][r] + bv1; v1 = v1 > 0.0f ? v1 : 0.01f * v1;
+                float v2 = acc2[m][n][r] + bv2; v2 = v2 > 0.0f ? v2 : 0.01f * v2;
+                float v = v1 + v2;
+                Yb[(size_t)row * 128 + col] = v;
+                lsum[n] += v;
+                lsq[n] = fmaf(v, v, lsq[n]);
+            }
+        }
+    __syncthreads();
+    float* ssum = reinterpret_cast<float*>(As);
+    float* ssq  = ssum + 128;
+    if (t < 128) { ssum[t] = 0.0f; ssq[t] = 0.0f; }
+    __syncthreads();
+    #pragma unroll
+    for (int n = 0; n < 4; ++n) {
+        int col = wc * 64 + n * 16 + fr;
+        atomicAdd(&ssum[col], lsum[n]);
+        atomicAdd(&ssq[col], lsq[n]);
+    }
+    __syncthreads();
+    if (t < 128) {
+        atomicAdd(&stats[t], ssum[t]);
+        atomicAdd(&stats[128 + t], ssq[t]);
+    }
 }
 
 __global__ __launch_bounds__(256) void bn_final(float* __restrict__ xs,
@@ -673,11 +720,7 @@
     int*    idxb  = (int*)ws;
     float*  wnb   = ws + 98304;
     float4* sposg = (float4*)(ws + 196608);
-    float*  x1    = ws + 196608 + 32768;
-    float*  PbC   = x1  + (size_t)B * NC * CH;
-    float*  QbC   = PbC + (size_t)B * NC * CH;
-    float*  aggC  = QbC + (size_t)B * NC * CH;
-    float*  stats = aggC+ (size_t)B * NC * CH;
+    float*  stats = ws + 196608 + 32768;
     int* cntC  = (int*)(stats + 256);
     int* cntF  = cntC + B * NC;
     int* cntZ  = cntF + B * NF;
@@ -700,36 +743,42 @@
     ushort* QSb   = PSb   + (size_t)B * NF * 128;
     ushort* agg2b = QSb   + (size_t)B * NF * 128;
     ushort* aggSb = agg2b + (size_t)B * NF * 128;
-    ushort* W2eT  = aggSb + (size_t)B * NF * 128;
+    ushort* xb16  = aggSb + (size_t)B * NF * 128;
+    ushort* PQc   = xb16  + (size_t)B * NC * 128;
+    ushort* aggCb = PQc   + (size_t)B * NC * 128;
+    ushort* x1b   = aggCb + (size_t)B * NC * 64;
+    ushort* W2eT  = x1b   + (size_t)B * NC * 64;
     ushort* W2nT  = W2eT  + 128 * 128;
     ushort* WseT  = W2nT  + 128 * 192;
     ushort* WsnT  = WseT  + 128 * 256;
+    ushort* W1eT  = WsnT  + 128 * 256;
+    ushort* W1nT  = W1eT  + 128 * 128;
 
     float* y  = (float*)d_out;
     float* wf = y + (size_t)B * NF * COUT;
 
     hipMemsetAsync(stats, 0, 256 * 4 + (size_t)B * (NC + NF + ZB) * 4, stream);
-    count_all<<<dim3(EF / 256, B, 4), 256, 0, stream>>>(
+    count_all<<<dim3(EF / 256, B, 6), 256, 0, stream>>>(
         ec, ef, mask, pos, cntC, cntF, cntZ, invm,
-        W2e, W2n, Wse, Wsn, W2eT, W2nT, WseT, WsnT);
+        W2e, W2n, Wse, Wsn, W2eT, W2nT, WseT, WsnT,
+        W1e, W1n, W1eT, W1nT, x, xb16);
     scan_all<<<dim3(3 * B), 1024, 0, stream>>>(cntC, offC, curC, cntF, offF, curF, cntZ, offZ, curZ);
     fill_all<<<dim3(EF / 256, B, 3), 256, 0, stream>>>(ec, ef, mask, pos, curC, curF, curZ,
                                                        csrC, csrF, sposg, invm);
 
-    knn_interp<<<dim3(NF / 8, B), 256, 0, stream>>>(pos, sposg, offZ, x, idxb, wnb, xupb);
-
-    gemm_pq64<<<dim3(NC / 64, 1, B * 2), 256, 0, stream>>>(x, W1e, PbC, QbC);
-    agg_csr_f32<<<dim3(NC / 4, B), 256, 0, stream>>>(
-        PbC, QbC, b1e, offC, cntC, csrC, aggC, NC, EC);
-    gemm_kernel<<<dim3(1, NC / 64, B), 256, 0, stream>>>(
-        x, CIN, aggC, CH, W1n, b1n, x1, NC, CH, 1, (long)NC * CIN, (long)NC * CH, (long)NC * CH);
-
-    interp_b16<4><<<dim3(NF / 16, B), 256, 0, stream>>>(x1, idxb, wnb, x1upb);
-
-    mfma_pq_fused<<<dim3(NF / 128, 1, B * 2), 256, 0, stream>>>(
-        x1upb, xupb, W2eT, WseT, P2b, Q2b, PSb, QSb);
-    agg_csr_b16<<<dim3((NF / 4) * B * 2), 256, 0, stream>>>(
-        P2b, Q2b, b2e, PSb, QSb, bse, offF, cntF, csrF, agg2b, aggSb);
+    knn_cpq<<<dim3(B * NC / 128 + B * NF / 8), 256, 0, stream>>>(
+        pos, sposg, offZ, x, idxb, wnb, xupb, xb16, W1eT, PQc);
+
+    pqs_aggc<<<dim3(B * NF / 128 + B * NC / 4), 256, 0, stream>>>(
+        xupb, WseT, PSb, QSb, PQc, b1e, offC, cntC, csrC, aggCb);
+
+    x1_aggs<<<dim3(B * NC / 256 + B * NF / 4), 256, 0, stream>>>(
+        xb16, aggCb, W1nT, b1n, x1b, PSb, QSb, bse, offF, cntF, csrF, aggSb);
+
+    interp_x1<<<dim3(NF / 16, B), 256, 0, stream>>>(x1b, idxb, wnb, x1upb);
+
+    pq2_kernel<<<dim3(B * NF / 128), 256, 0, stream>>>(x1upb, W2eT, P2b, Q2b);
+    agg2_kernel<<<dim3(B * NF / 4), 256, 0, stream>>>(P2b, Q2b, b2e, offF, cntF, csrF, agg2b);
 
     mfma_node2<<<dim3(NF / 128, 1, B), 256, 0, stream>>>(
         x1upb, agg2b, W2nT, b2n, xupb, aggSb, WsnT, bsn, y, stats);
```

Result: slower. 240.0 us (+21.1%).
